# Kernel optimization log

Hardware: AMD Instinct MI355X
Metric: run time of the kernel (lower is better)

Reference implementation:

```python
import jax, jax.numpy as jnp
from jax import lax
import numpy as np

ALPHA = 2.0
EROSIONS = 10


def setup_inputs() -> dict:
    key = jax.random.key(0)
    k1, k2 = jax.random.split(key)
    b, c, h, w = 32, 1, 1024, 1024
    pred = jax.random.uniform(k1, (b, c, h, w), dtype=jnp.float32)
    target = jax.random.randint(k2, (b, c, h, w), 0, 2, dtype=jnp.int32)
    return {"pred": pred, "target": target}


def _perform_erosion(bound, kernel, alpha, erosions):
    # bound: (b, 1, H, W); kernel: (1, 1, 3, 3) cross * 0.2
    def step(carry, k):
        bnd, eroted = carry
        dilation = lax.conv_general_dilated(bnd, kernel, window_strides=(1, 1), padding="SAME")
        erosion = jnp.maximum(dilation - 0.5, 0.0)
        # per-sample global max/min over channel+spatial dims
        emax = jnp.max(erosion, axis=(1, 2, 3), keepdims=True)
        emin = jnp.min(erosion, axis=(1, 2, 3), keepdims=True)
        denom = emax - emin
        safe = jnp.where(denom != 0, denom, jnp.ones_like(denom))
        erosion = jnp.where(denom != 0, (erosion - emin) / safe, erosion)
        eroted = eroted + erosion * (k + 1.0) ** alpha
        return (erosion, eroted), None

    init = (bound, jnp.zeros_like(bound))
    (_, eroted), _ = lax.scan(step, init, jnp.arange(erosions, dtype=bound.dtype))
    return eroted


def reference(pred, target):
    # cross-shaped 3x3 erosion kernel scaled by 0.2 (fixed buffer)
    cross = jnp.array([[0.0, 1.0, 0.0], [1.0, 1.0, 1.0], [0.0, 1.0, 0.0]], dtype=pred.dtype) * 0.2
    kernel = cross[None, None]  # (1, 1, 3, 3)
    c = pred.shape[1]
    losses = []
    for i in range(c):
        tgt = (target == i).astype(pred.dtype)  # (b, c, H, W); c==1 here
        bound = (pred[:, i : i + 1] - tgt) ** 2
        eroted = _perform_erosion(bound, kernel, ALPHA, EROSIONS)
        losses.append(jnp.mean(eroted))
    return jnp.mean(jnp.stack(losses))
```

## Files before the change

kernel.cpp:

```cpp
#include <hip/hip_runtime.h>
#include <hip/hip_fp16.h>

#define BATCH 32
#define H 1024
#define W 1024
#define NPIX (H * W)
#define ITERS 10
#define SROWS 16
#define BROWS 32
#define STRIPS (H / BROWS)

typedef _Float16 half8_t __attribute__((ext_vector_type(8)));

struct Stats {
    unsigned maxbits[ITERS][BATCH];
    unsigned minbits[ITERS][BATCH];
    double   sum[ITERS][BATCH];
};

__global__ void init_stats(Stats* st) {
    int i = blockIdx.x * blockDim.x + threadIdx.x;
    if (i < ITERS * BATCH) {
        (&st->maxbits[0][0])[i] = 0u;
        (&st->minbits[0][0])[i] = 0x7f800000u;
        (&st->sum[0][0])[i]     = 0.0;
    }
}

__device__ __forceinline__ float bound1(const float* __restrict__ pred,
                                        const int* __restrict__ tgt, size_t off) {
    float d = pred[off] - (tgt[off] == 0 ? 1.f : 0.f);
    return d * d;
}

template <int MODE>
__device__ __forceinline__ void row_load8(
    const float* __restrict__ pred, const int* __restrict__ target,
    const _Float16* __restrict__ in, size_t base, int r, int lane128,
    float emin, float invd, float f[8], float& L, float& R)
{
    const int  col = lane128 * 8;
    const bool inb = (r >= 0) && (r < H);
    size_t off = base + (size_t)r * W + col;
    if (inb) {
        if (MODE == 0) {
            float4 p0 = *(const float4*)(pred + off);
            float4 p1 = *(const float4*)(pred + off + 4);
            int4   t0 = *(const int4*)(target + off);
            int4   t1 = *(const int4*)(target + off + 4);
            float d;
            d = p0.x - (t0.x == 0 ? 1.f : 0.f); f[0] = d * d;
            d = p0.y - (t0.y == 0 ? 1.f : 0.f); f[1] = d * d;
            d = p0.z - (t0.z == 0 ? 1.f : 0.f); f[2] = d * d;
            d = p0.w - (t0.w == 0 ? 1.f : 0.f); f[3] = d * d;
            d = p1.x - (t1.x == 0 ? 1.f : 0.f); f[4] = d * d;
            d = p1.y - (t1.y == 0 ? 1.f : 0.f); f[5] = d * d;
            d = p1.z - (t1.z == 0 ? 1.f : 0.f); f[6] = d * d;
            d = p1.w - (t1.w == 0 ? 1.f : 0.f); f[7] = d * d;
        } else {
            half8_t x = *(const half8_t*)(in + off);
            #pragma unroll
            for (int j = 0; j < 8; ++j)
                f[j] = ((float)x[j] - emin) * invd;
        }
    } else {
        #pragma unroll
        for (int j = 0; j < 8; ++j) f[j] = 0.f;
    }

    L = __shfl_up(f[7], 1, 64);
    R = __shfl_down(f[0], 1, 64);

    const int wl = lane128 & 63;
    if (!inb) { L = 0.f; R = 0.f; return; }
    if (lane128 == 0) {
        L = 0.f;
    } else if (wl == 0) {
        size_t o = off - 1;
        L = (MODE == 0) ? bound1(pred, target, o)
                        : ((float)in[o] - emin) * invd;
    }
    if (lane128 == 127) {
        R = 0.f;
    } else if (wl == 63) {
        size_t o = off + 8;
        R = (MODE == 0) ? bound1(pred, target, o)
                        : ((float)in[o] - emin) * invd;
    }
}

template <int MODE, int STORE>
__global__ __launch_bounds__(256) void erode_strip(
    const float* __restrict__ pred, const int* __restrict__ target,
    const _Float16* __restrict__ in, _Float16* __restrict__ out,
    Stats* __restrict__ st, int iter)
{
    const int blk = blockIdx.x;
    const int b   = blk >> 5;
    const int s   = blk & (STRIPS - 1);
    const int tid = threadIdx.x;
    const int sub     = tid >> 7;
    const int lane128 = tid & 127;
    const int r0  = s * BROWS + sub * SROWS;
    const int col = lane128 * 8;
    const size_t base = (size_t)b * NPIX;

    float emin = 0.f, invd = 1.f;
    if (MODE == 1) {
        float emax = __uint_as_float(st->maxbits[iter - 1][b]);
        float emn  = __uint_as_float(st->minbits[iter - 1][b]);
        float denom = emax - emn;
        if (denom != 0.f) { emin = emn; invd = 1.f / denom; }
    }

    float prev[8], cur[8], nxt[8];
    float Lp, Rp, Lc, Rc, Ln, Rn;
    row_load8<MODE>(pred, target, in, base, r0 - 1, lane128, emin, invd, prev, Lp, Rp);
    row_load8<MODE>(pred, target, in, base, r0,     lane128, emin, invd, cur,  Lc, Rc);

    float  m  = 0.f;
    float  mn = __builtin_inf();
    double sum = 0.0;

    #pragma unroll 2
    for (int i = 0; i < SROWS; ++i) {
        const int r = r0 + i;
        row_load8<MODE>(pred, target, in, base, r + 1, lane128, emin, invd, nxt, Ln, Rn);

        float e[8];
        #pragma unroll
        for (int j = 0; j < 8; ++j) {
            float lf = (j == 0) ? Lc : cur[j - 1];
            float rf = (j == 7) ? Rc : cur[j + 1];
            e[j] = fmaxf(0.2f * (cur[j] + lf + rf + prev[j] + nxt[j]) - 0.5f, 0.f);
        }

        if (STORE) {
            half8_t o;
            #pragma unroll
            for (int j = 0; j < 8; ++j) o[j] = (_Float16)e[j];
            *(half8_t*)(out + base + (size_t)r * W + col) = o;
        }

        float rm = fmaxf(fmaxf(fmaxf(e[0], e[1]), fmaxf(e[2], e[3])),
                         fmaxf(fmaxf(e[4], e[5]), fmaxf(e[6], e[7])));
        float rn = fminf(fminf(fminf(e[0], e[1]), fminf(e[2], e[3])),
                         fminf(fminf(e[4], e[5]), fminf(e[6], e[7])));
        float rs = ((e[0] + e[1]) + (e[2] + e[3])) + ((e[4] + e[5]) + (e[6] + e[7]));
        m   = fmaxf(m, rm);
        mn  = fminf(mn, rn);
        sum += (double)rs;

        #pragma unroll
        for (int j = 0; j < 8; ++j) { prev[j] = cur[j]; cur[j] = nxt[j]; }
        Lc = Ln; Rc = Rn;
    }

    #pragma unroll
    for (int off = 32; off > 0; off >>= 1) {
        m   = fmaxf(m,  __shfl_down(m,  off, 64));
        mn  = fminf(mn, __shfl_down(mn, off, 64));
        sum += __shfl_down(sum, off, 64);
    }
    __shared__ float  smax[4];
    __shared__ float  smin[4];
    __shared__ double ssum[4];
    int lane = tid & 63, wave = tid >> 6;
    if (lane == 0) { smax[wave] = m; smin[wave] = mn; ssum[wave] = sum; }
    __syncthreads();
    if (tid == 0) {
        m   = fmaxf(fmaxf(smax[0], smax[1]), fmaxf(smax[2], smax[3]));
        mn  = fminf(fminf(smin[0], smin[1]), fminf(smin[2], smin[3]));
        sum = ssum[0] + ssum[1] + ssum[2] + ssum[3];
        atomicMax(&st->maxbits[iter][b], __float_as_uint(m));
        atomicMin(&st->minbits[iter][b], __float_as_uint(mn));
        atomicAdd(&st->sum[iter][b], sum);
    }
}

__global__ void finalize(const Stats* __restrict__ st, float* __restrict__ out) {
    if (threadIdx.x == 0 && blockIdx.x == 0) {
        double total = 0.0;
        for (int k = 0; k < ITERS; ++k) {
            double w = (double)((k + 1) * (k + 1));
            for (int b = 0; b < BATCH; ++b) {
                float emax  = __uint_as_float(st->maxbits[k][b]);
                float emn   = __uint_as_float(st->minbits[k][b]);
                float denom = emax - emn;
                double s = st->sum[k][b];
                double sn;
                if (denom != 0.f)
                    sn = (s - (double)NPIX * (double)emn) / (double)denom;
                else
                    sn = s;
                total += w * sn;
            }
        }
        out[0] = (float)(total / ((double)BATCH * (double)NPIX));
    }
}

extern "C" void kernel_launch(void* const* d_in, const int* in_sizes, int n_in,
                              void* d_out, int out_size, void* d_ws, size_t ws_size,
                              hipStream_t stream) {
    (void)in_sizes; (void)n_in; (void)out_size;
    const float* pred   = (const float*)d_in[0];
    const int*   target = (const int*)d_in[1];

    const size_t fieldBytes = (size_t)BATCH * NPIX * sizeof(_Float16);
    char* ws = (char*)d_ws;
    _Float16* bufA;
    _Float16* bufB;
    Stats* st;
    if (ws_size >= 2 * fieldBytes + sizeof(Stats)) {
        bufA = (_Float16*)ws;
        bufB = (_Float16*)(ws + fieldBytes);
        st   = (Stats*)(ws + 2 * fieldBytes);
    } else {
        bufA = (_Float16*)ws;
        bufB = (_Float16*)d_in[1];
        st   = (Stats*)(ws + fieldBytes);
    }

    init_stats<<<1, 320, 0, stream>>>(st);

    dim3 grid(BATCH * STRIPS), block(256);
    erode_strip<0, 1><<<grid, block, 0, stream>>>(pred, target, nullptr, bufA, st, 0);

    _Float16* src = bufA;
    _Float16* dst = bufB;
    for (int k = 1; k < ITERS; ++k) {
        if (k == ITERS - 1)
            erode_strip<1, 0><<<grid, block, 0, stream>>>(nullptr, nullptr, src, dst, st, k);
        else
            erode_strip<1, 1><<<grid, block, 0, stream>>>(nullptr, nullptr, src, dst, st, k);
        _Float16* t = src; src = dst; dst = t;
    }

    finalize<<<1, 64, 0, stream>>>(st, (float*)d_out);
}
```

Measured before the change: 575.3 us.

## Software-pipeline row loads with double-buffered raw registers and halve strip height

```diff
diff --git a/kernel.cpp b/kernel.cpp
--- a/kernel.cpp
+++ b/kernel.cpp
@@ -6,9 +6,10 @@
 #define W 1024
 #define NPIX (H * W)
 #define ITERS 10
-#define SROWS 16
-#define BROWS 32
+#define SROWS 8
+#define BROWS 16
 #define STRIPS (H / BROWS)
+#define TOTAL_STRIPS (BATCH * STRIPS)
 
 typedef _Float16 half8_t __attribute__((ext_vector_type(8)));
 
@@ -27,111 +28,125 @@
     }
 }
 
-__device__ __forceinline__ float bound1(const float* __restrict__ pred,
-                                        const int* __restrict__ tgt, size_t off) {
-    float d = pred[off] - (tgt[off] == 0 ? 1.f : 0.f);
+__device__ __forceinline__ float bsq(float p, int t) {
+    float d = p - (t == 0 ? 1.f : 0.f);
     return d * d;
 }
 
+template <int MODE> struct Raw;
+template <> struct Raw<0> { float4 p0, p1; int4 t0, t1; float pL, pR; int tL, tR; };
+template <> struct Raw<1> { half8_t x; _Float16 xL, xR; };
+
 template <int MODE>
-__device__ __forceinline__ void row_load8(
-    const float* __restrict__ pred, const int* __restrict__ target,
-    const _Float16* __restrict__ in, size_t base, int r, int lane128,
-    float emin, float invd, float f[8], float& L, float& R)
-{
-    const int  col = lane128 * 8;
+__device__ __forceinline__ void issue_row(const float* __restrict__ pred,
+    const int* __restrict__ target, const _Float16* __restrict__ in,
+    size_t base, int r, int lane128, Raw<MODE>& raw)
+{
     const bool inb = (r >= 0) && (r < H);
-    size_t off = base + (size_t)r * W + col;
-    if (inb) {
-        if (MODE == 0) {
-            float4 p0 = *(const float4*)(pred + off);
-            float4 p1 = *(const float4*)(pred + off + 4);
-            int4   t0 = *(const int4*)(target + off);
-            int4   t1 = *(const int4*)(target + off + 4);
-            float d;
-            d = p0.x - (t0.x == 0 ? 1.f : 0.f); f[0] = d * d;
-            d = p0.y - (t0.y == 0 ? 1.f : 0.f); f[1] = d * d;
-            d = p0.z - (t0.z == 0 ? 1.f : 0.f); f[2] = d * d;
-            d = p0.w - (t0.w == 0 ? 1.f : 0.f); f[3] = d * d;
-            d = p1.x - (t1.x == 0 ? 1.f : 0.f); f[4] = d * d;
-            d = p1.y - (t1.y == 0 ? 1.f : 0.f); f[5] = d * d;
-            d = p1.z - (t1.z == 0 ? 1.f : 0.f); f[6] = d * d;
-            d = p1.w - (t1.w == 0 ? 1.f : 0.f); f[7] = d * d;
-        } else {
-            half8_t x = *(const half8_t*)(in + off);
-            #pragma unroll
-            for (int j = 0; j < 8; ++j)
-                f[j] = ((float)x[j] - emin) * invd;
-        }
+    if (!inb) return;
+    const int wl = lane128 & 63;
+    const size_t off = base + (size_t)r * W + (size_t)(lane128 * 8);
+    if constexpr (MODE == 0) {
+        raw.p0 = *(const float4*)(pred + off);
+        raw.p1 = *(const float4*)(pred + off + 4);
+        raw.t0 = *(const int4*)(target + off);
+        raw.t1 = *(const int4*)(target + off + 4);
+        if (wl == 0 && lane128 != 0)    { raw.pL = pred[off - 1]; raw.tL = target[off - 1]; }
+        if (wl == 63 && lane128 != 127) { raw.pR = pred[off + 8]; raw.tR = target[off + 8]; }
     } else {
+        raw.x = *(const half8_t*)(in + off);
+        if (wl == 0 && lane128 != 0)    raw.xL = in[off - 1];
+        if (wl == 63 && lane128 != 127) raw.xR = in[off + 8];
+    }
+}
+
+template <int MODE>
+__device__ __forceinline__ void convert_row(int r, int lane128,
+    float emin, float invd, const Raw<MODE>& raw,
+    float f[8], float& eL, float& eR)
+{
+    const bool inb = (r >= 0) && (r < H);
+    const int wl = lane128 & 63;
+    if (!inb) {
         #pragma unroll
         for (int j = 0; j < 8; ++j) f[j] = 0.f;
-    }
-
-    L = __shfl_up(f[7], 1, 64);
-    R = __shfl_down(f[0], 1, 64);
-
-    const int wl = lane128 & 63;
-    if (!inb) { L = 0.f; R = 0.f; return; }
-    if (lane128 == 0) {
-        L = 0.f;
-    } else if (wl == 0) {
-        size_t o = off - 1;
-        L = (MODE == 0) ? bound1(pred, target, o)
-                        : ((float)in[o] - emin) * invd;
-    }
-    if (lane128 == 127) {
-        R = 0.f;
-    } else if (wl == 63) {
-        size_t o = off + 8;
-        R = (MODE == 0) ? bound1(pred, target, o)
-                        : ((float)in[o] - emin) * invd;
+        eL = 0.f; eR = 0.f;
+        return;
+    }
+    if constexpr (MODE == 0) {
+        f[0] = bsq(raw.p0.x, raw.t0.x); f[1] = bsq(raw.p0.y, raw.t0.y);
+        f[2] = bsq(raw.p0.z, raw.t0.z); f[3] = bsq(raw.p0.w, raw.t0.w);
+        f[4] = bsq(raw.p1.x, raw.t1.x); f[5] = bsq(raw.p1.y, raw.t1.y);
+        f[6] = bsq(raw.p1.z, raw.t1.z); f[7] = bsq(raw.p1.w, raw.t1.w);
+        eL = (wl == 0 && lane128 != 0)    ? bsq(raw.pL, raw.tL) : 0.f;
+        eR = (wl == 63 && lane128 != 127) ? bsq(raw.pR, raw.tR) : 0.f;
+    } else {
+        #pragma unroll
+        for (int j = 0; j < 8; ++j) f[j] = ((float)raw.x[j] - emin) * invd;
+        eL = (wl == 0 && lane128 != 0)    ? ((float)raw.xL - emin) * invd : 0.f;
+        eR = (wl == 63 && lane128 != 127) ? ((float)raw.xR - emin) * invd : 0.f;
     }
 }
 
 template <int MODE, int STORE>
-__global__ __launch_bounds__(256) void erode_strip(
+__device__ __forceinline__ void do_strip(
     const float* __restrict__ pred, const int* __restrict__ target,
     const _Float16* __restrict__ in, _Float16* __restrict__ out,
-    Stats* __restrict__ st, int iter)
-{
-    const int blk = blockIdx.x;
-    const int b   = blk >> 5;
-    const int s   = blk & (STRIPS - 1);
-    const int tid = threadIdx.x;
+    Stats* __restrict__ st, int iter, int strip, int tid)
+{
+    const int b   = strip >> 6;
+    const int s   = strip & (STRIPS - 1);
     const int sub     = tid >> 7;
     const int lane128 = tid & 127;
+    const int wl      = lane128 & 63;
     const int r0  = s * BROWS + sub * SROWS;
     const int col = lane128 * 8;
     const size_t base = (size_t)b * NPIX;
 
     float emin = 0.f, invd = 1.f;
     if (MODE == 1) {
-        float emax = __uint_as_float(st->maxbits[iter - 1][b]);
-        float emn  = __uint_as_float(st->minbits[iter - 1][b]);
+        float emax  = __uint_as_float(st->maxbits[iter - 1][b]);
+        float emn   = __uint_as_float(st->minbits[iter - 1][b]);
         float denom = emax - emn;
         if (denom != 0.f) { emin = emn; invd = 1.f / denom; }
     }
 
+    Raw<MODE> rA, rB;
     float prev[8], cur[8], nxt[8];
-    float Lp, Rp, Lc, Rc, Ln, Rn;
-    row_load8<MODE>(pred, target, in, base, r0 - 1, lane128, emin, invd, prev, Lp, Rp);
-    row_load8<MODE>(pred, target, in, base, r0,     lane128, emin, invd, cur,  Lc, Rc);
+    float eLc, eRc, eLn, eRn, dL, dR;
+
+    issue_row<MODE>(pred, target, in, base, r0 - 1, lane128, rA);
+    issue_row<MODE>(pred, target, in, base, r0,     lane128, rB);
+    convert_row<MODE>(r0 - 1, lane128, emin, invd, rA, prev, dL, dR);
+    convert_row<MODE>(r0,     lane128, emin, invd, rB, cur, eLc, eRc);
+    issue_row<MODE>(pred, target, in, base, r0 + 1, lane128, rA);
 
     float  m  = 0.f;
     float  mn = __builtin_inf();
     double sum = 0.0;
 
-    #pragma unroll 2
+    #pragma unroll
     for (int i = 0; i < SROWS; ++i) {
         const int r = r0 + i;
-        row_load8<MODE>(pred, target, in, base, r + 1, lane128, emin, invd, nxt, Ln, Rn);
+        if (i < SROWS - 1) {
+            if (i & 1) issue_row<MODE>(pred, target, in, base, r + 2, lane128, rA);
+            else       issue_row<MODE>(pred, target, in, base, r + 2, lane128, rB);
+        }
+        if (i & 1) convert_row<MODE>(r + 1, lane128, emin, invd, rB, nxt, eLn, eRn);
+        else       convert_row<MODE>(r + 1, lane128, emin, invd, rA, nxt, eLn, eRn);
+
+        float L = __shfl_up(cur[7], 1, 64);
+        float R = __shfl_down(cur[0], 1, 64);
+        if (lane128 == 0)   L = 0.f;
+        else if (wl == 0)   L = eLc;
+        if (lane128 == 127) R = 0.f;
+        else if (wl == 63)  R = eRc;
 
         float e[8];
         #pragma unroll
         for (int j = 0; j < 8; ++j) {
-            float lf = (j == 0) ? Lc : cur[j - 1];
-            float rf = (j == 7) ? Rc : cur[j + 1];
+            float lf = (j == 0) ? L : cur[j - 1];
+            float rf = (j == 7) ? R : cur[j + 1];
             e[j] = fmaxf(0.2f * (cur[j] + lf + rf + prev[j] + nxt[j]) - 0.5f, 0.f);
         }
 
@@ -153,7 +168,7 @@
 
         #pragma unroll
         for (int j = 0; j < 8; ++j) { prev[j] = cur[j]; cur[j] = nxt[j]; }
-        Lc = Ln; Rc = Rn;
+        eLc = eLn; eRc = eRn;
     }
 
     #pragma unroll
@@ -165,7 +180,7 @@
     __shared__ float  smax[4];
     __shared__ float  smin[4];
     __shared__ double ssum[4];
-    int lane = tid & 63, wave = tid >> 6;
+    const int lane = tid & 63, wave = tid >> 6;
     if (lane == 0) { smax[wave] = m; smin[wave] = mn; ssum[wave] = sum; }
     __syncthreads();
     if (tid == 0) {
@@ -176,6 +191,21 @@
         atomicMin(&st->minbits[iter][b], __float_as_uint(mn));
         atomicAdd(&st->sum[iter][b], sum);
     }
+}
+
+__global__ __launch_bounds__(256, 6) void erode0(
+    const float* __restrict__ pred, const int* __restrict__ target,
+    _Float16* __restrict__ out, Stats* __restrict__ st)
+{
+    do_strip<0, 1>(pred, target, nullptr, out, st, 0, blockIdx.x, threadIdx.x);
+}
+
+template <int STORE>
+__global__ __launch_bounds__(256, 8) void erode1(
+    const _Float16* __restrict__ in, _Float16* __restrict__ out,
+    Stats* __restrict__ st, int iter)
+{
+    do_strip<1, STORE>(nullptr, nullptr, in, out, st, iter, blockIdx.x, threadIdx.x);
 }
 
 __global__ void finalize(const Stats* __restrict__ st, float* __restrict__ out) {
@@ -224,16 +254,16 @@
 
     init_stats<<<1, 320, 0, stream>>>(st);
 
-    dim3 grid(BATCH * STRIPS), block(256);
-    erode_strip<0, 1><<<grid, block, 0, stream>>>(pred, target, nullptr, bufA, st, 0);
+    dim3 grid(TOTAL_STRIPS), block(256);
+    erode0<<<grid, block, 0, stream>>>(pred, target, bufA, st);
 
     _Float16* src = bufA;
     _Float16* dst = bufB;
     for (int k = 1; k < ITERS; ++k) {
         if (k == ITERS - 1)
-            erode_strip<1, 0><<<grid, block, 0, stream>>>(nullptr, nullptr, src, dst, st, k);
+            erode1<0><<<grid, block, 0, stream>>>(src, nullptr, st, k);
         else
-            erode_strip<1, 1><<<grid, block, 0, stream>>>(nullptr, nullptr, src, dst, st, k);
+            erode1<1><<<grid, block, 0, stream>>>(src, dst, st, k);
         _Float16* t = src; src = dst; dst = t;
     }
 
```

Measured after the change: 867.8 us. 50.8% more time.

## Stage fp16 erosion rows through LDS ring with async global-to-LDS loads

Applied to the files above, without the earlier changes.

```diff
diff --git a/kernel.cpp b/kernel.cpp
--- a/kernel.cpp
+++ b/kernel.cpp
@@ -6,11 +6,18 @@
 #define W 1024
 #define NPIX (H * W)
 #define ITERS 10
+
 #define SROWS 16
 #define BROWS 32
 #define STRIPS (H / BROWS)
 
+#define G1 8
+#define RING 4
+
 typedef _Float16 half8_t __attribute__((ext_vector_type(8)));
+
+#define AS1 __attribute__((address_space(1)))
+#define AS3 __attribute__((address_space(3)))
 
 struct Stats {
     unsigned maxbits[ITERS][BATCH];
@@ -33,36 +40,27 @@
     return d * d;
 }
 
-template <int MODE>
 __device__ __forceinline__ void row_load8(
     const float* __restrict__ pred, const int* __restrict__ target,
-    const _Float16* __restrict__ in, size_t base, int r, int lane128,
-    float emin, float invd, float f[8], float& L, float& R)
+    size_t base, int r, int lane128, float f[8], float& L, float& R)
 {
     const int  col = lane128 * 8;
     const bool inb = (r >= 0) && (r < H);
     size_t off = base + (size_t)r * W + col;
     if (inb) {
-        if (MODE == 0) {
-            float4 p0 = *(const float4*)(pred + off);
-            float4 p1 = *(const float4*)(pred + off + 4);
-            int4   t0 = *(const int4*)(target + off);
-            int4   t1 = *(const int4*)(target + off + 4);
-            float d;
-            d = p0.x - (t0.x == 0 ? 1.f : 0.f); f[0] = d * d;
-            d = p0.y - (t0.y == 0 ? 1.f : 0.f); f[1] = d * d;
-            d = p0.z - (t0.z == 0 ? 1.f : 0.f); f[2] = d * d;
-            d = p0.w - (t0.w == 0 ? 1.f : 0.f); f[3] = d * d;
-            d = p1.x - (t1.x == 0 ? 1.f : 0.f); f[4] = d * d;
-            d = p1.y - (t1.y == 0 ? 1.f : 0.f); f[5] = d * d;
-            d = p1.z - (t1.z == 0 ? 1.f : 0.f); f[6] = d * d;
-            d = p1.w - (t1.w == 0 ? 1.f : 0.f); f[7] = d * d;
-        } else {
-            half8_t x = *(const half8_t*)(in + off);
-            #pragma unroll
-            for (int j = 0; j < 8; ++j)
-                f[j] = ((float)x[j] - emin) * invd;
-        }
+        float4 p0 = *(const float4*)(pred + off);
+        float4 p1 = *(const float4*)(pred + off + 4);
+        int4   t0 = *(const int4*)(target + off);
+        int4   t1 = *(const int4*)(target + off + 4);
+        float d;
+        d = p0.x - (t0.x == 0 ? 1.f : 0.f); f[0] = d * d;
+        d = p0.y - (t0.y == 0 ? 1.f : 0.f); f[1] = d * d;
+        d = p0.z - (t0.z == 0 ? 1.f : 0.f); f[2] = d * d;
+        d = p0.w - (t0.w == 0 ? 1.f : 0.f); f[3] = d * d;
+        d = p1.x - (t1.x == 0 ? 1.f : 0.f); f[4] = d * d;
+        d = p1.y - (t1.y == 0 ? 1.f : 0.f); f[5] = d * d;
+        d = p1.z - (t1.z == 0 ? 1.f : 0.f); f[6] = d * d;
+        d = p1.w - (t1.w == 0 ? 1.f : 0.f); f[7] = d * d;
     } else {
         #pragma unroll
         for (int j = 0; j < 8; ++j) f[j] = 0.f;
@@ -73,27 +71,15 @@
 
     const int wl = lane128 & 63;
     if (!inb) { L = 0.f; R = 0.f; return; }
-    if (lane128 == 0) {
-        L = 0.f;
-    } else if (wl == 0) {
-        size_t o = off - 1;
-        L = (MODE == 0) ? bound1(pred, target, o)
-                        : ((float)in[o] - emin) * invd;
-    }
-    if (lane128 == 127) {
-        R = 0.f;
-    } else if (wl == 63) {
-        size_t o = off + 8;
-        R = (MODE == 0) ? bound1(pred, target, o)
-                        : ((float)in[o] - emin) * invd;
-    }
-}
-
-template <int MODE, int STORE>
-__global__ __launch_bounds__(256) void erode_strip(
+    if (lane128 == 0)        L = 0.f;
+    else if (wl == 0)        L = bound1(pred, target, off - 1);
+    if (lane128 == 127)      R = 0.f;
+    else if (wl == 63)       R = bound1(pred, target, off + 8);
+}
+
+__global__ __launch_bounds__(256) void erode0(
     const float* __restrict__ pred, const int* __restrict__ target,
-    const _Float16* __restrict__ in, _Float16* __restrict__ out,
-    Stats* __restrict__ st, int iter)
+    _Float16* __restrict__ out, Stats* __restrict__ st)
 {
     const int blk = blockIdx.x;
     const int b   = blk >> 5;
@@ -105,18 +91,10 @@
     const int col = lane128 * 8;
     const size_t base = (size_t)b * NPIX;
 
-    float emin = 0.f, invd = 1.f;
-    if (MODE == 1) {
-        float emax = __uint_as_float(st->maxbits[iter - 1][b]);
-        float emn  = __uint_as_float(st->minbits[iter - 1][b]);
-        float denom = emax - emn;
-        if (denom != 0.f) { emin = emn; invd = 1.f / denom; }
-    }
-
     float prev[8], cur[8], nxt[8];
     float Lp, Rp, Lc, Rc, Ln, Rn;
-    row_load8<MODE>(pred, target, in, base, r0 - 1, lane128, emin, invd, prev, Lp, Rp);
-    row_load8<MODE>(pred, target, in, base, r0,     lane128, emin, invd, cur,  Lc, Rc);
+    row_load8(pred, target, base, r0 - 1, lane128, prev, Lp, Rp);
+    row_load8(pred, target, base, r0,     lane128, cur,  Lc, Rc);
 
     float  m  = 0.f;
     float  mn = __builtin_inf();
@@ -125,7 +103,7 @@
     #pragma unroll 2
     for (int i = 0; i < SROWS; ++i) {
         const int r = r0 + i;
-        row_load8<MODE>(pred, target, in, base, r + 1, lane128, emin, invd, nxt, Ln, Rn);
+        row_load8(pred, target, base, r + 1, lane128, nxt, Ln, Rn);
 
         float e[8];
         #pragma unroll
@@ -135,12 +113,10 @@
             e[j] = fmaxf(0.2f * (cur[j] + lf + rf + prev[j] + nxt[j]) - 0.5f, 0.f);
         }
 
-        if (STORE) {
-            half8_t o;
-            #pragma unroll
-            for (int j = 0; j < 8; ++j) o[j] = (_Float16)e[j];
-            *(half8_t*)(out + base + (size_t)r * W + col) = o;
-        }
+        half8_t o;
+        #pragma unroll
+        for (int j = 0; j < 8; ++j) o[j] = (_Float16)e[j];
+        *(half8_t*)(out + base + (size_t)r * W + col) = o;
 
         float rm = fmaxf(fmaxf(fmaxf(e[0], e[1]), fmaxf(e[2], e[3])),
                          fmaxf(fmaxf(e[4], e[5]), fmaxf(e[6], e[7])));
@@ -172,6 +148,128 @@
         m   = fmaxf(fmaxf(smax[0], smax[1]), fmaxf(smax[2], smax[3]));
         mn  = fminf(fminf(smin[0], smin[1]), fminf(smin[2], smin[3]));
         sum = ssum[0] + ssum[1] + ssum[2] + ssum[3];
+        atomicMax(&st->maxbits[0][b], __float_as_uint(m));
+        atomicMin(&st->minbits[0][b], __float_as_uint(mn));
+        atomicAdd(&st->sum[0][b], sum);
+    }
+}
+
+template <int STORE>
+__global__ __launch_bounds__(256, 4) void erode1(
+    const _Float16* __restrict__ in, _Float16* __restrict__ out,
+    Stats* __restrict__ st, int iter)
+{
+    __shared__ _Float16 ring[4][RING][W];
+    const int tid  = threadIdx.x;
+    const int wv   = tid >> 6;
+    const int lane = tid & 63;
+    const int blk  = blockIdx.x;
+    const int b    = blk >> 5;
+    const int s    = blk & (STRIPS - 1);
+    const int r0   = s * BROWS + wv * G1;
+    const size_t base = (size_t)b * NPIX;
+
+    float emin = 0.f, invd = 1.f;
+    {
+        float emax  = __uint_as_float(st->maxbits[iter - 1][b]);
+        float emn   = __uint_as_float(st->minbits[iter - 1][b]);
+        float denom = emax - emn;
+        if (denom != 0.f) { emin = emn; invd = 1.f / denom; }
+    }
+
+    auto issue = [&](int r) {
+        const int rc = r < 0 ? 0 : (r >= H ? H - 1 : r);
+        const _Float16* g = in + base + (size_t)rc * W + lane * 8;
+        _Float16* l = &ring[wv][r & (RING - 1)][0];
+        __builtin_amdgcn_global_load_lds((const AS1 void*)g,         (AS3 void*)l,         16, 0, 0);
+        __builtin_amdgcn_global_load_lds((const AS1 void*)(g + 512), (AS3 void*)(l + 512), 16, 0, 0);
+    };
+
+    auto convert = [&](int r, float f[16], float& L, float& R) {
+        if (r < 0 || r >= H) {
+            #pragma unroll
+            for (int j = 0; j < 16; ++j) f[j] = 0.f;
+            L = 0.f; R = 0.f;
+            return;
+        }
+        const _Float16* p = &ring[wv][r & (RING - 1)][0];
+        half8_t a = *(const half8_t*)(p + lane * 16);
+        half8_t c = *(const half8_t*)(p + lane * 16 + 8);
+        #pragma unroll
+        for (int j = 0; j < 8; ++j) {
+            f[j]     = ((float)a[j] - emin) * invd;
+            f[8 + j] = ((float)c[j] - emin) * invd;
+        }
+        L = (lane == 0)  ? 0.f : ((float)p[lane * 16 - 1]  - emin) * invd;
+        R = (lane == 63) ? 0.f : ((float)p[lane * 16 + 16] - emin) * invd;
+    };
+
+    issue(r0 - 1);
+    issue(r0);
+    issue(r0 + 1);
+    asm volatile("s_waitcnt vmcnt(2)" ::: "memory");
+    __builtin_amdgcn_sched_barrier(0);
+
+    float prev[16], cur[16], nxt[16];
+    float Lc, Rc, Ln, Rn, dL, dR;
+    convert(r0 - 1, prev, dL, dR);
+    convert(r0,     cur,  Lc, Rc);
+
+    float  m  = 0.f;
+    float  mn = __builtin_inf();
+    double sum = 0.0;
+
+    #pragma unroll
+    for (int i = 0; i < G1; ++i) {
+        const int r = r0 + i;
+        issue(r + 2);
+        if (STORE && i > 0) asm volatile("s_waitcnt vmcnt(4)" ::: "memory");
+        else                asm volatile("s_waitcnt vmcnt(2)" ::: "memory");
+        __builtin_amdgcn_sched_barrier(0);
+
+        convert(r + 1, nxt, Ln, Rn);
+
+        float e[16];
+        #pragma unroll
+        for (int j = 0; j < 16; ++j) {
+            float lf = (j == 0)  ? Lc : cur[j - 1];
+            float rf = (j == 15) ? Rc : cur[j + 1];
+            e[j] = fmaxf(0.2f * (cur[j] + lf + rf + prev[j] + nxt[j]) - 0.5f, 0.f);
+        }
+
+        if (STORE) {
+            half8_t o0, o1;
+            #pragma unroll
+            for (int j = 0; j < 8; ++j) { o0[j] = (_Float16)e[j]; o1[j] = (_Float16)e[8 + j]; }
+            _Float16* dst = out + base + (size_t)r * W + lane * 16;
+            *(half8_t*)dst       = o0;
+            *(half8_t*)(dst + 8) = o1;
+        }
+
+        float rm = e[0], rn = e[0], rs = e[0];
+        #pragma unroll
+        for (int j = 1; j < 16; ++j) {
+            rm = fmaxf(rm, e[j]);
+            rn = fminf(rn, e[j]);
+            rs += e[j];
+        }
+        m   = fmaxf(m, rm);
+        mn  = fminf(mn, rn);
+        sum += (double)rs;
+
+        #pragma unroll
+        for (int j = 0; j < 16; ++j) { prev[j] = cur[j]; cur[j] = nxt[j]; }
+        Lc = Ln; Rc = Rn;
+        __builtin_amdgcn_sched_barrier(0);
+    }
+
+    #pragma unroll
+    for (int off = 32; off > 0; off >>= 1) {
+        m   = fmaxf(m,  __shfl_down(m,  off, 64));
+        mn  = fminf(mn, __shfl_down(mn, off, 64));
+        sum += __shfl_down(sum, off, 64);
+    }
+    if (lane == 0) {
         atomicMax(&st->maxbits[iter][b], __float_as_uint(m));
         atomicMin(&st->minbits[iter][b], __float_as_uint(mn));
         atomicAdd(&st->sum[iter][b], sum);
@@ -225,15 +323,15 @@
     init_stats<<<1, 320, 0, stream>>>(st);
 
     dim3 grid(BATCH * STRIPS), block(256);
-    erode_strip<0, 1><<<grid, block, 0, stream>>>(pred, target, nullptr, bufA, st, 0);
+    erode0<<<grid, block, 0, stream>>>(pred, target, bufA, st);
 
     _Float16* src = bufA;
     _Float16* dst = bufB;
     for (int k = 1; k < ITERS; ++k) {
         if (k == ITERS - 1)
-            erode_strip<1, 0><<<grid, block, 0, stream>>>(nullptr, nullptr, src, dst, st, k);
+            erode1<0><<<grid, block, 0, stream>>>(src, nullptr, st, k);
         else
-            erode_strip<1, 1><<<grid, block, 0, stream>>>(nullptr, nullptr, src, dst, st, k);
+            erode1<1><<<grid, block, 0, stream>>>(src, dst, st, k);
         _Float16* t = src; src = dst; dst = t;
     }
 
```

Measured after the change: 903.2 us. +57.0%, slower.
